# Optimization experiments

Hardware: AMD Instinct MI355X
Metric: run time of the kernel (lower is better)

## Reference

```python
import jax, jax.numpy as jnp
import numpy as np

N_NODES = 50000
N_EDGES = 800000
N_FEAT = 256


def setup_inputs() -> dict:
    key = jax.random.key(0)
    k_h, k_src, k_dst, k_w1, k_w2 = jax.random.split(key, 5)
    h = jax.random.normal(k_h, (N_NODES, N_FEAT), dtype=jnp.float32)
    src = jax.random.randint(k_src, (N_EDGES,), 0, N_NODES, dtype=jnp.int32)
    dst = jax.random.randint(k_dst, (N_EDGES,), 0, N_NODES, dtype=jnp.int32)
    # Kaiming-uniform-ish init like nn.Linear defaults
    b1 = 1.0 / np.sqrt(2 * N_FEAT)
    b2 = 1.0 / np.sqrt(N_FEAT)
    W1_w = jax.random.uniform(k_w1, (N_FEAT, 2 * N_FEAT), dtype=jnp.float32, minval=-b1, maxval=b1)
    W1_b = jnp.zeros((N_FEAT,), dtype=jnp.float32)
    W2_w = jax.random.uniform(k_w2, (1, N_FEAT), dtype=jnp.float32, minval=-b2, maxval=b2)
    W2_b = jnp.zeros((1,), dtype=jnp.float32)
    return {"h": h, "src": src, "dst": dst, "W1_w": W1_w, "W1_b": W1_b, "W2_w": W2_w, "W2_b": W2_b}


def reference(h, src, dst, W1_w, W1_b, W2_w, W2_b):
    # Gather per-edge endpoint features and concat along feature dim: [E, 2F]
    e = jnp.concatenate([h[src], h[dst]], axis=-1)
    # 2-layer MLP: Linear -> ReLU -> Linear, squeeze to per-edge score [E]
    hid = jax.nn.relu(e @ W1_w.T + W1_b)          # [E, F]
    score = (hid @ W2_w.T + W2_b)[:, 0]            # [E]
    return score
```

## Files before the change

### kernel.cpp

```cpp
#include <hip/hip_runtime.h>

#define F 256
#define TWO_F 512
#define BM 128
#define BN 128
#define BK 64
#define ASTR 72

typedef __attribute__((ext_vector_type(8))) short short8;
typedef __attribute__((ext_vector_type(4))) float float4v;

static __device__ __forceinline__ unsigned short f2bf(float f) {
    unsigned u = __float_as_uint(f);
    u += 0x7FFFu + ((u >> 16) & 1u);
    return (unsigned short)(u >> 16);
}
static __device__ __forceinline__ unsigned pack2(float lo, float hi) {
    unsigned a = __float_as_uint(lo) + 0x8000u;
    unsigned b = __float_as_uint(hi) + 0x8000u;
    return __builtin_amdgcn_perm(b, a, 0x07060302u);
}
static __device__ __forceinline__ float blo(unsigned u) { return __uint_as_float(u << 16); }
static __device__ __forceinline__ float rawf(unsigned u) { return __uint_as_float(u); }

__global__ void prep_w_kernel(const float* __restrict__ W1, unsigned short* __restrict__ Wb) {
    int i = blockIdx.x * blockDim.x + threadIdx.x;
    if (i >= TWO_F * F) return;
    int n = i >> 8;
    int k = i & 255;
    float v = W1[(n & 255) * TWO_F + ((n >> 8) << 8) + k];
    int kin_sw = ((k & 63) + (n & 7) * 8) & 63;
    Wb[n * F + (k & ~63) + kin_sw] = f2bf(v);
}

__global__ __launch_bounds__(256, 3) void gemm_kernel(
    const float* __restrict__ h, const unsigned short* __restrict__ Wb,
    const float* __restrict__ b1v, unsigned short* __restrict__ C, int M)
{
    __shared__ unsigned short sA[BM * ASTR];
    __shared__ unsigned short sB[BN * BK];

    const int ib = blockIdx.x;
    const int r8 = ib & 7;
    const int q  = ib >> 3;
    const int by = q & 3;
    const int bx = (q >> 2) * 8 + r8;
    const int bm = bx * BM;
    if (bm >= M) return;
    const int bn = by * BN;

    const int tid  = threadIdx.x;
    const int lane = tid & 63;
    const int wid  = tid >> 6;
    const int wm   = wid >> 1;
    const int wn   = wid & 1;

    const int ar = tid >> 1;
    const int ak = (tid & 1) * 32;
    int arow = bm + ar; if (arow > M - 1) arow = M - 1;
    const float* hrow = h + (size_t)arow * F + ak;

    const int brow0 = wid * 32;
    const int b_r   = lane >> 3;
    const int b_k   = (lane & 7) * 8;

    float4v acc[4][4];
    #pragma unroll
    for (int i = 0; i < 4; ++i)
        #pragma unroll
        for (int j = 0; j < 4; ++j) acc[i][j] = (float4v)(0.f);

    const int quad = lane >> 4;
    const int l15  = lane & 15;
    const int ksw  = (l15 & 7) * 8;

    for (int k0 = 0; k0 < F; k0 += BK) {
        #pragma unroll
        for (int p = 0; p < 4; ++p) {
            int r = brow0 + p * 8;
            const unsigned short* gp = Wb + (size_t)(bn + r + b_r) * F + k0 + b_k;
            __builtin_amdgcn_global_load_lds(
                (const __attribute__((address_space(1))) unsigned int*)gp,
                (__attribute__((address_space(3))) unsigned int*)&sB[r * BK],
                16, 0, 0);
        }

        const float* p = hrow + k0;
        #pragma unroll
        for (int half = 0; half < 2; ++half) {
            float4 a0 = *(const float4*)(p + half * 16 + 0);
            float4 a1 = *(const float4*)(p + half * 16 + 4);
            float4 a2 = *(const float4*)(p + half * 16 + 8);
            float4 a3 = *(const float4*)(p + half * 16 + 12);
            uint4 q0, q1;
            q0.x = pack2(a0.x, a0.y); q0.y = pack2(a0.z, a0.w);
            q0.z = pack2(a1.x, a1.y); q0.w = pack2(a1.z, a1.w);
            q1.x = pack2(a2.x, a2.y); q1.y = pack2(a2.z, a2.w);
            q1.z = pack2(a3.x, a3.y); q1.w = pack2(a3.z, a3.w);
            *(uint4*)&sA[ar * ASTR + ak + half * 16 + 0] = q0;
            *(uint4*)&sA[ar * ASTR + ak + half * 16 + 8] = q1;
        }
        __syncthreads();

        #pragma unroll
        for (int ks = 0; ks < 2; ++ks) {
            short8 afr[4], bfr[4];
            #pragma unroll
            for (int mt = 0; mt < 4; ++mt)
                afr[mt] = *(const short8*)&sA[(wm * 64 + mt * 16 + l15) * ASTR + ks * 32 + quad * 8];
            #pragma unroll
            for (int nt = 0; nt < 4; ++nt) {
                int koff = (ks * 32 + quad * 8 + ksw) & 63;
                bfr[nt] = *(const short8*)&sB[(wn * 64 + nt * 16 + l15) * BK + koff];
            }
            #pragma unroll
            for (int mt = 0; mt < 4; ++mt)
                #pragma unroll
                for (int nt = 0; nt < 4; ++nt)
                    acc[mt][nt] = __builtin_amdgcn_mfma_f32_16x16x32_bf16(
                        afr[mt], bfr[nt], acc[mt][nt], 0, 0, 0);
        }
        __syncthreads();
    }

    float bias[4];
    #pragma unroll
    for (int nt = 0; nt < 4; ++nt) {
        int n = bn + wn * 64 + nt * 16 + l15;
        bias[nt] = (n < F) ? b1v[n] : 0.f;
    }
    #pragma unroll
    for (int mt = 0; mt < 4; ++mt) {
        int gm0 = bm + wm * 64 + mt * 16 + quad * 4;
        #pragma unroll
        for (int rr = 0; rr < 4; ++rr) {
            int gm = gm0 + rr;
            if (gm < M) {
                unsigned short* cp = C + (size_t)gm * TWO_F + bn + wn * 64 + l15;
                #pragma unroll
                for (int nt = 0; nt < 4; ++nt)
                    cp[nt * 16] = f2bf(acc[mt][nt][rr] + bias[nt]);
            }
        }
    }
}

__global__ __launch_bounds__(256) void edge_kernel(
    const unsigned short* __restrict__ C,
    const int* __restrict__ src, const int* __restrict__ dst,
    const float* __restrict__ w2,
    const float* __restrict__ b2, float* __restrict__ out, int E)
{
    const int lane = threadIdx.x & 31;
    const int g = blockIdx.x * 8 + (threadIdx.x >> 5);
    const int e0 = g * 2;
    if (e0 >= E) return;
    const int s0 = src[e0], d0 = dst[e0];
    const int s1 = src[e0 + 1], d1 = dst[e0 + 1];

    uint4 av0 = *(const uint4*)(C + (size_t)s0 * TWO_F + lane * 8);
    uint4 bv0 = *(const uint4*)(C + (size_t)d0 * TWO_F + F + lane * 8);
    uint4 av1 = *(const uint4*)(C + (size_t)s1 * TWO_F + lane * 8);
    uint4 bv1 = *(const uint4*)(C + (size_t)d1 * TWO_F + F + lane * 8);
    float4 w0 = *(const float4*)(w2 + lane * 8);
    float4 w1 = *(const float4*)(w2 + lane * 8 + 4);

    float sum0, sum1;
    sum0  = w0.x * fmaxf(blo(av0.x) + blo(bv0.x), 0.f);
    sum0 += w0.y * fmaxf(rawf(av0.x) + rawf(bv0.x), 0.f);
    sum0 += w0.z * fmaxf(blo(av0.y) + blo(bv0.y), 0.f);
    sum0 += w0.w * fmaxf(rawf(av0.y) + rawf(bv0.y), 0.f);
    sum0 += w1.x * fmaxf(blo(av0.z) + blo(bv0.z), 0.f);
    sum0 += w1.y * fmaxf(rawf(av0.z) + rawf(bv0.z), 0.f);
    sum0 += w1.z * fmaxf(blo(av0.w) + blo(bv0.w), 0.f);
    sum0 += w1.w * fmaxf(rawf(av0.w) + rawf(bv0.w), 0.f);

    sum1  = w0.x * fmaxf(blo(av1.x) + blo(bv1.x), 0.f);
    sum1 += w0.y * fmaxf(rawf(av1.x) + rawf(bv1.x), 0.f);
    sum1 += w0.z * fmaxf(blo(av1.y) + blo(bv1.y), 0.f);
    sum1 += w0.w * fmaxf(rawf(av1.y) + rawf(bv1.y), 0.f);
    sum1 += w1.x * fmaxf(blo(av1.z) + blo(bv1.z), 0.f);
    sum1 += w1.y * fmaxf(rawf(av1.z) + rawf(bv1.z), 0.f);
    sum1 += w1.z * fmaxf(blo(av1.w) + blo(bv1.w), 0.f);
    sum1 += w1.w * fmaxf(rawf(av1.w) + rawf(bv1.w), 0.f);

    #pragma unroll
    for (int off = 16; off > 0; off >>= 1) {
        sum0 += __shfl_down(sum0, off, 32);
        sum1 += __shfl_down(sum1, off, 32);
    }

    if (lane == 0) {
        float b = b2[0];
        out[e0]     = sum0 + b;
        out[e0 + 1] = sum1 + b;
    }
}

extern "C" void kernel_launch(void* const* d_in, const int* in_sizes, int n_in,
                              void* d_out, int out_size, void* d_ws, size_t ws_size,
                              hipStream_t stream) {
    const float* h    = (const float*)d_in[0];
    const int*   src  = (const int*)d_in[1];
    const int*   dst  = (const int*)d_in[2];
    const float* W1_w = (const float*)d_in[3];
    const float* W1_b = (const float*)d_in[4];
    const float* W2_w = (const float*)d_in[5];
    const float* W2_b = (const float*)d_in[6];
    float* out = (float*)d_out;

    const int M = in_sizes[0] / F;
    const int E = in_sizes[1];

    unsigned short* Wb = (unsigned short*)d_ws;
    unsigned short* C  = (unsigned short*)((char*)d_ws + 512 * 1024);

    prep_w_kernel<<<(TWO_F * F + 255) / 256, 256, 0, stream>>>(W1_w, Wb);

    int nbx = ((M + BM - 1) / BM + 7) / 8 * 8;
    gemm_kernel<<<nbx * 4, 256, 0, stream>>>(h, Wb, W1_b, C, M);

    edge_kernel<<<(E / 2 + 7) / 8, 256, 0, stream>>>(C, src, dst, W2_w, W2_b, out, E);
}
```

Before: 241.3 us.

## Pre-convert h to swizzled bf16 and load A tiles via global_load_lds; widen edge batching

Adds a prep kernel that converts h to bf16 in a swizzled layout, so the GEMM can stream A tiles straight into LDS with global_load_lds like B, instead of loading fp32 into registers, packing and storing to LDS on every iteration. The edge kernel now handles four edges per 32-lane group, with vectorized index loads and a float4 output store, so more gathers are in flight. The cost is an extra kernel launch plus a full fp32 read and bf16 write of h, and the four-edge vector access assumes E is a multiple of 4.

```diff
diff --git a/kernel.cpp b/kernel.cpp
--- a/kernel.cpp
+++ b/kernel.cpp
@@ -5,7 +5,6 @@
 #define BM 128
 #define BN 128
 #define BK 64
-#define ASTR 72
 
 typedef __attribute__((ext_vector_type(8))) short short8;
 typedef __attribute__((ext_vector_type(4))) float float4v;
@@ -33,11 +32,24 @@
     Wb[n * F + (k & ~63) + kin_sw] = f2bf(v);
 }
 
+__global__ __launch_bounds__(256) void prep_h_kernel(
+    const float* __restrict__ h, unsigned short* __restrict__ hb, int M)
+{
+    int i = blockIdx.x * blockDim.x + threadIdx.x;
+    if (i >= M * 128) return;
+    int m = i >> 7;
+    int kp = (i & 127) * 2;
+    float2 v = *(const float2*)(h + (size_t)m * F + kp);
+    unsigned pk = pack2(v.x, v.y);
+    int ksw = ((kp & 63) + (m & 7) * 8) & 63;
+    *(unsigned*)(hb + (size_t)m * F + (kp & ~63) + ksw) = pk;
+}
+
 __global__ __launch_bounds__(256, 3) void gemm_kernel(
-    const float* __restrict__ h, const unsigned short* __restrict__ Wb,
+    const unsigned short* __restrict__ hb, const unsigned short* __restrict__ Wb,
     const float* __restrict__ b1v, unsigned short* __restrict__ C, int M)
 {
-    __shared__ unsigned short sA[BM * ASTR];
+    __shared__ unsigned short sA[BM * BK];
     __shared__ unsigned short sB[BN * BK];
 
     const int ib = blockIdx.x;
@@ -55,14 +67,9 @@
     const int wm   = wid >> 1;
     const int wn   = wid & 1;
 
-    const int ar = tid >> 1;
-    const int ak = (tid & 1) * 32;
-    int arow = bm + ar; if (arow > M - 1) arow = M - 1;
-    const float* hrow = h + (size_t)arow * F + ak;
-
-    const int brow0 = wid * 32;
-    const int b_r   = lane >> 3;
-    const int b_k   = (lane & 7) * 8;
+    const int row0 = wid * 32;
+    const int st_r = lane >> 3;
+    const int st_k = (lane & 7) * 8;
 
     float4v acc[4][4];
     #pragma unroll
@@ -72,47 +79,36 @@
 
     const int quad = lane >> 4;
     const int l15  = lane & 15;
-    const int ksw  = (l15 & 7) * 8;
+    const int rot  = (l15 & 7) * 8;
 
     for (int k0 = 0; k0 < F; k0 += BK) {
         #pragma unroll
         for (int p = 0; p < 4; ++p) {
-            int r = brow0 + p * 8;
-            const unsigned short* gp = Wb + (size_t)(bn + r + b_r) * F + k0 + b_k;
+            int r = row0 + p * 8;
+            int am = bm + r + st_r; if (am > M - 1) am = M - 1;
+            const unsigned short* ga = hb + (size_t)am * F + k0 + st_k;
             __builtin_amdgcn_global_load_lds(
-                (const __attribute__((address_space(1))) unsigned int*)gp,
+                (const __attribute__((address_space(1))) unsigned int*)ga,
+                (__attribute__((address_space(3))) unsigned int*)&sA[r * BK],
+                16, 0, 0);
+            const unsigned short* gb = Wb + (size_t)(bn + r + st_r) * F + k0 + st_k;
+            __builtin_amdgcn_global_load_lds(
+                (const __attribute__((address_space(1))) unsigned int*)gb,
                 (__attribute__((address_space(3))) unsigned int*)&sB[r * BK],
                 16, 0, 0);
         }
-
-        const float* p = hrow + k0;
-        #pragma unroll
-        for (int half = 0; half < 2; ++half) {
-            float4 a0 = *(const float4*)(p + half * 16 + 0);
-            float4 a1 = *(const float4*)(p + half * 16 + 4);
-            float4 a2 = *(const float4*)(p + half * 16 + 8);
-            float4 a3 = *(const float4*)(p + half * 16 + 12);
-            uint4 q0, q1;
-            q0.x = pack2(a0.x, a0.y); q0.y = pack2(a0.z, a0.w);
-            q0.z = pack2(a1.x, a1.y); q0.w = pack2(a1.z, a1.w);
-            q1.x = pack2(a2.x, a2.y); q1.y = pack2(a2.z, a2.w);
-            q1.z = pack2(a3.x, a3.y); q1.w = pack2(a3.z, a3.w);
-            *(uint4*)&sA[ar * ASTR + ak + half * 16 + 0] = q0;
-            *(uint4*)&sA[ar * ASTR + ak + half * 16 + 8] = q1;
-        }
         __syncthreads();
 
         #pragma unroll
         for (int ks = 0; ks < 2; ++ks) {
+            const int koff = (ks * 32 + quad * 8 + rot) & 63;
             short8 afr[4], bfr[4];
             #pragma unroll
             for (int mt = 0; mt < 4; ++mt)
-                afr[mt] = *(const short8*)&sA[(wm * 64 + mt * 16 + l15) * ASTR + ks * 32 + quad * 8];
+                afr[mt] = *(const short8*)&sA[(wm * 64 + mt * 16 + l15) * BK + koff];
             #pragma unroll
-            for (int nt = 0; nt < 4; ++nt) {
-                int koff = (ks * 32 + quad * 8 + ksw) & 63;
+            for (int nt = 0; nt < 4; ++nt)
                 bfr[nt] = *(const short8*)&sB[(wn * 64 + nt * 16 + l15) * BK + koff];
-            }
             #pragma unroll
             for (int mt = 0; mt < 4; ++mt)
                 #pragma unroll
@@ -153,47 +149,52 @@
 {
     const int lane = threadIdx.x & 31;
     const int g = blockIdx.x * 8 + (threadIdx.x >> 5);
-    const int e0 = g * 2;
+    const int e0 = g * 4;
     if (e0 >= E) return;
-    const int s0 = src[e0], d0 = dst[e0];
-    const int s1 = src[e0 + 1], d1 = dst[e0 + 1];
-
-    uint4 av0 = *(const uint4*)(C + (size_t)s0 * TWO_F + lane * 8);
-    uint4 bv0 = *(const uint4*)(C + (size_t)d0 * TWO_F + F + lane * 8);
-    uint4 av1 = *(const uint4*)(C + (size_t)s1 * TWO_F + lane * 8);
-    uint4 bv1 = *(const uint4*)(C + (size_t)d1 * TWO_F + F + lane * 8);
+    int4 sv = *(const int4*)(src + e0);
+    int4 dv = *(const int4*)(dst + e0);
+
+    const unsigned short* Ca = C + lane * 8;
+    const unsigned short* Cb = C + F + lane * 8;
+    uint4 a0 = *(const uint4*)(Ca + (size_t)sv.x * TWO_F);
+    uint4 b0 = *(const uint4*)(Cb + (size_t)dv.x * TWO_F);
+    uint4 a1 = *(const uint4*)(Ca + (size_t)sv.y * TWO_F);
+    uint4 b1 = *(const uint4*)(Cb + (size_t)dv.y * TWO_F);
+    uint4 a2 = *(const uint4*)(Ca + (size_t)sv.z * TWO_F);
+    uint4 b2v = *(const uint4*)(Cb + (size_t)dv.z * TWO_F);
+    uint4 a3 = *(const uint4*)(Ca + (size_t)sv.w * TWO_F);
+    uint4 b3 = *(const uint4*)(Cb + (size_t)dv.w * TWO_F);
     float4 w0 = *(const float4*)(w2 + lane * 8);
     float4 w1 = *(const float4*)(w2 + lane * 8 + 4);
 
-    float sum0, sum1;
-    sum0  = w0.x * fmaxf(blo(av0.x) + blo(bv0.x), 0.f);
-    sum0 += w0.y * fmaxf(rawf(av0.x) + rawf(bv0.x), 0.f);
-    sum0 += w0.z * fmaxf(blo(av0.y) + blo(bv0.y), 0.f);
-    sum0 += w0.w * fmaxf(rawf(av0.y) + rawf(bv0.y), 0.f);
-    sum0 += w1.x * fmaxf(blo(av0.z) + blo(bv0.z), 0.f);
-    sum0 += w1.y * fmaxf(rawf(av0.z) + rawf(bv0.z), 0.f);
-    sum0 += w1.z * fmaxf(blo(av0.w) + blo(bv0.w), 0.f);
-    sum0 += w1.w * fmaxf(rawf(av0.w) + rawf(bv0.w), 0.f);
-
-    sum1  = w0.x * fmaxf(blo(av1.x) + blo(bv1.x), 0.f);
-    sum1 += w0.y * fmaxf(rawf(av1.x) + rawf(bv1.x), 0.f);
-    sum1 += w0.z * fmaxf(blo(av1.y) + blo(bv1.y), 0.f);
-    sum1 += w0.w * fmaxf(rawf(av1.y) + rawf(bv1.y), 0.f);
-    sum1 += w1.x * fmaxf(blo(av1.z) + blo(bv1.z), 0.f);
-    sum1 += w1.y * fmaxf(rawf(av1.z) + rawf(bv1.z), 0.f);
-    sum1 += w1.z * fmaxf(blo(av1.w) + blo(bv1.w), 0.f);
-    sum1 += w1.w * fmaxf(rawf(av1.w) + rawf(bv1.w), 0.f);
+#define ESUM(s, av, bv)                                   \
+    s  = w0.x * fmaxf(blo(av.x) + blo(bv.x), 0.f);        \
+    s += w0.y * fmaxf(rawf(av.x) + rawf(bv.x), 0.f);      \
+    s += w0.z * fmaxf(blo(av.y) + blo(bv.y), 0.f);        \
+    s += w0.w * fmaxf(rawf(av.y) + rawf(bv.y), 0.f);      \
+    s += w1.x * fmaxf(blo(av.z) + blo(bv.z), 0.f);        \
+    s += w1.y * fmaxf(rawf(av.z) + rawf(bv.z), 0.f);      \
+    s += w1.z * fmaxf(blo(av.w) + blo(bv.w), 0.f);        \
+    s += w1.w * fmaxf(rawf(av.w) + rawf(bv.w), 0.f);
+
+    float sum0, sum1, sum2, sum3;
+    ESUM(sum0, a0, b0)
+    ESUM(sum1, a1, b1)
+    ESUM(sum2, a2, b2v)
+    ESUM(sum3, a3, b3)
+#undef ESUM
 
     #pragma unroll
     for (int off = 16; off > 0; off >>= 1) {
         sum0 += __shfl_down(sum0, off, 32);
         sum1 += __shfl_down(sum1, off, 32);
+        sum2 += __shfl_down(sum2, off, 32);
+        sum3 += __shfl_down(sum3, off, 32);
     }
 
     if (lane == 0) {
         float b = b2[0];
-        out[e0]     = sum0 + b;
-        out[e0 + 1] = sum1 + b;
+        *(float4*)(out + e0) = make_float4(sum0 + b, sum1 + b, sum2 + b, sum3 + b);
     }
 }
 
@@ -213,12 +214,14 @@
     const int E = in_sizes[1];
 
     unsigned short* Wb = (unsigned short*)d_ws;
-    unsigned short* C  = (unsigned short*)((char*)d_ws + 512 * 1024);
+    unsigned short* hb = (unsigned short*)((char*)d_ws + 512 * 1024);
+    unsigned short* C  = (unsigned short*)((char*)d_ws + 512 * 1024 + 26 * 1024 * 1024);
 
     prep_w_kernel<<<(TWO_F * F + 255) / 256, 256, 0, stream>>>(W1_w, Wb);
+    prep_h_kernel<<<(M * 128 + 255) / 256, 256, 0, stream>>>(h, hb, M);
 
     int nbx = ((M + BM - 1) / BM + 7) / 8 * 8;
-    gemm_kernel<<<nbx * 4, 256, 0, stream>>>(h, Wb, W1_b, C, M);
-
-    edge_kernel<<<(E / 2 + 7) / 8, 256, 0, stream>>>(C, src, dst, W2_w, W2_b, out, E);
-}
+    gemm_kernel<<<nbx * 4, 256, 0, stream>>>(hb, Wb, W1_b, C, M);
+
+    edge_kernel<<<(E / 4 + 7) / 8, 256, 0, stream>>>(C, src, dst, W2_w, W2_b, out, E);
+}
```

Result: faster. 230.4 us (-4.5%).

## Hold weight tile in registers and stream A from global without LDS

Applied to the files above, without the earlier changes.

The GEMM kernel drops its shared-memory tiling. Each wave now keeps its full 64-column by 256-K slice of bf16 weights in registers (32 short8 fragments) and walks eight 16-row M tiles. It reads h directly from global memory into MFMA A-fragments with no barriers. The grid shrinks to two N-halves per 128-row chunk, and the weight prep no longer swizzles. This removes LDS traffic and syncs, at the cost of heavy register pressure (launch bounds reduced to 2), redundant h reads across the four waves, and lower occupancy.

```diff
diff --git a/kernel.cpp b/kernel.cpp
--- a/kernel.cpp
+++ b/kernel.cpp
@@ -2,10 +2,6 @@
 
 #define F 256
 #define TWO_F 512
-#define BM 128
-#define BN 128
-#define BK 64
-#define ASTR 72
 
 typedef __attribute__((ext_vector_type(8))) short short8;
 typedef __attribute__((ext_vector_type(4))) float float4v;
@@ -28,118 +24,71 @@
     if (i >= TWO_F * F) return;
     int n = i >> 8;
     int k = i & 255;
-    float v = W1[(n & 255) * TWO_F + ((n >> 8) << 8) + k];
-    int kin_sw = ((k & 63) + (n & 7) * 8) & 63;
-    Wb[n * F + (k & ~63) + kin_sw] = f2bf(v);
+    Wb[i] = f2bf(W1[(n & 255) * TWO_F + ((n >> 8) << 8) + k]);
 }
 
-__global__ __launch_bounds__(256, 3) void gemm_kernel(
+__global__ __launch_bounds__(256, 2) void gemm_kernel(
     const float* __restrict__ h, const unsigned short* __restrict__ Wb,
     const float* __restrict__ b1v, unsigned short* __restrict__ C, int M)
 {
-    __shared__ unsigned short sA[BM * ASTR];
-    __shared__ unsigned short sB[BN * BK];
+    const int tid  = threadIdx.x;
+    const int lane = tid & 63;
+    const int wv   = tid >> 6;
+    const int quad = lane >> 4;
+    const int l15  = lane & 15;
 
     const int ib = blockIdx.x;
-    const int r8 = ib & 7;
-    const int q  = ib >> 3;
-    const int by = q & 3;
-    const int bx = (q >> 2) * 8 + r8;
-    const int bm = bx * BM;
-    if (bm >= M) return;
-    const int bn = by * BN;
+    const int mchunk = (ib >> 4) * 8 + (ib & 7);
+    const int by = (ib >> 3) & 1;
+    const int m0 = mchunk * 128;
+    if (m0 >= M) return;
+    const int nbase = by * 256 + wv * 64;
 
-    const int tid  = threadIdx.x;
-    const int lane = tid & 63;
-    const int wid  = tid >> 6;
-    const int wm   = wid >> 1;
-    const int wn   = wid & 1;
-
-    const int ar = tid >> 1;
-    const int ak = (tid & 1) * 32;
-    int arow = bm + ar; if (arow > M - 1) arow = M - 1;
-    const float* hrow = h + (size_t)arow * F + ak;
-
-    const int brow0 = wid * 32;
-    const int b_r   = lane >> 3;
-    const int b_k   = (lane & 7) * 8;
-
-    float4v acc[4][4];
+    short8 bfr[4][8];
     #pragma unroll
-    for (int i = 0; i < 4; ++i)
+    for (int nt = 0; nt < 4; ++nt) {
+        const unsigned short* bp = Wb + (size_t)(nbase + nt * 16 + l15) * F + quad * 8;
         #pragma unroll
-        for (int j = 0; j < 4; ++j) acc[i][j] = (float4v)(0.f);
-
-    const int quad = lane >> 4;
-    const int l15  = lane & 15;
-    const int ksw  = (l15 & 7) * 8;
-
-    for (int k0 = 0; k0 < F; k0 += BK) {
-        #pragma unroll
-        for (int p = 0; p < 4; ++p) {
-            int r = brow0 + p * 8;
-            const unsigned short* gp = Wb + (size_t)(bn + r + b_r) * F + k0 + b_k;
-            __builtin_amdgcn_global_load_lds(
-                (const __attribute__((address_space(1))) unsigned int*)gp,
-                (__attribute__((address_space(3))) unsigned int*)&sB[r * BK],
-                16, 0, 0);
-        }
-
-        const float* p = hrow + k0;
-        #pragma unroll
-        for (int half = 0; half < 2; ++half) {
-            float4 a0 = *(const float4*)(p + half * 16 + 0);
-            float4 a1 = *(const float4*)(p + half * 16 + 4);
-            float4 a2 = *(const float4*)(p + half * 16 + 8);
-            float4 a3 = *(const float4*)(p + half * 16 + 12);
-            uint4 q0, q1;
-            q0.x = pack2(a0.x, a0.y); q0.y = pack2(a0.z, a0.w);
-            q0.z = pack2(a1.x, a1.y); q0.w = pack2(a1.z, a1.w);
-            q1.x = pack2(a2.x, a2.y); q1.y = pack2(a2.z, a2.w);
-            q1.z = pack2(a3.x, a3.y); q1.w = pack2(a3.z, a3.w);
-            *(uint4*)&sA[ar * ASTR + ak + half * 16 + 0] = q0;
-            *(uint4*)&sA[ar * ASTR + ak + half * 16 + 8] = q1;
-        }
-        __syncthreads();
-
-        #pragma unroll
-        for (int ks = 0; ks < 2; ++ks) {
-            short8 afr[4], bfr[4];
-            #pragma unroll
-            for (int mt = 0; mt < 4; ++mt)
-                afr[mt] = *(const short8*)&sA[(wm * 64 + mt * 16 + l15) * ASTR + ks * 32 + quad * 8];
-            #pragma unroll
-            for (int nt = 0; nt < 4; ++nt) {
-                int koff = (ks * 32 + quad * 8 + ksw) & 63;
-                bfr[nt] = *(const short8*)&sB[(wn * 64 + nt * 16 + l15) * BK + koff];
-            }
-            #pragma unroll
-            for (int mt = 0; mt < 4; ++mt)
-                #pragma unroll
-                for (int nt = 0; nt < 4; ++nt)
-                    acc[mt][nt] = __builtin_amdgcn_mfma_f32_16x16x32_bf16(
-                        afr[mt], bfr[nt], acc[mt][nt], 0, 0, 0);
-        }
-        __syncthreads();
+        for (int ks = 0; ks < 8; ++ks)
+            bfr[nt][ks] = *(const short8*)(bp + ks * 32);
     }
 
     float bias[4];
     #pragma unroll
-    for (int nt = 0; nt < 4; ++nt) {
-        int n = bn + wn * 64 + nt * 16 + l15;
-        bias[nt] = (n < F) ? b1v[n] : 0.f;
-    }
-    #pragma unroll
-    for (int mt = 0; mt < 4; ++mt) {
-        int gm0 = bm + wm * 64 + mt * 16 + quad * 4;
+    for (int nt = 0; nt < 4; ++nt)
+        bias[nt] = (by == 0) ? b1v[nbase + nt * 16 + l15] : 0.f;
+
+    for (int t = 0; t < 8; ++t) {
+        const int mt0 = m0 + t * 16;
+        int arow = mt0 + l15; if (arow > M - 1) arow = M - 1;
+        const float* ap = h + (size_t)arow * F + quad * 8;
+
+        float4v acc[4];
+        acc[0] = acc[1] = acc[2] = acc[3] = (float4v)(0.f);
+
         #pragma unroll
-        for (int rr = 0; rr < 4; ++rr) {
-            int gm = gm0 + rr;
+        for (int ks = 0; ks < 8; ++ks) {
+            float4 lo = *(const float4*)(ap + ks * 32);
+            float4 hi = *(const float4*)(ap + ks * 32 + 4);
+            union { unsigned u[4]; short8 s; } a;
+            a.u[0] = pack2(lo.x, lo.y);
+            a.u[1] = pack2(lo.z, lo.w);
+            a.u[2] = pack2(hi.x, hi.y);
+            a.u[3] = pack2(hi.z, hi.w);
+            #pragma unroll
+            for (int nt = 0; nt < 4; ++nt)
+                acc[nt] = __builtin_amdgcn_mfma_f32_16x16x32_bf16(
+                    a.s, bfr[nt][ks], acc[nt], 0, 0, 0);
+        }
+
+        #pragma unroll
+        for (int r = 0; r < 4; ++r) {
+            int gm = mt0 + quad * 4 + r;
             if (gm < M) {
-                unsigned short* cp = C + (size_t)gm * TWO_F + bn + wn * 64 + l15;
+                unsigned short* cp = C + (size_t)gm * TWO_F + nbase + l15;
                 #pragma unroll
                 for (int nt = 0; nt < 4; ++nt)
-                    cp[nt * 16] = f2bf(acc[mt][nt][rr] + bias[nt]);
+                    cp[nt * 16] = f2bf(acc[nt][r] + bias[nt]);
             }
         }
     }
@@ -217,8 +166,8 @@
 
     prep_w_kernel<<<(TWO_F * F + 255) / 256, 256, 0, stream>>>(W1_w, Wb);
 
-    int nbx = ((M + BM - 1) / BM + 7) / 8 * 8;
-    gemm_kernel<<<nbx * 4, 256, 0, stream>>>(h, Wb, W1_b, C, M);
+    int nchunks = ((M + 127) / 128 + 7) / 8 * 8;
+    gemm_kernel<<<nchunks * 2, 256, 0, stream>>>(h, Wb, W1_b, C, M);
 
     edge_kernel<<<(E / 2 + 7) / 8, 256, 0, stream>>>(C, src, dst, W2_w, W2_b, out, E);
 }
```

Measured after the change: 274.5 us. 13.8% more time.

## Pre-convert h to swizzled bf16 and stream A tiles via direct global-to-LDS loads

Applied to the files above, without the earlier changes.

A prep kernel now converts h to bf16 in a swizzled layout alongside the weight preparation. The GEMM then loads both A and B tiles with global_load_lds instead of doing fp32 loads and an in-register conversion per tile. The N tile shrinks from 128 to 64 with occupancy raised to 4, so each block computes a smaller tile and the grid doubles. The aim is to cut A-side conversion overhead and raise occupancy, at the cost of an extra round trip of h through memory and re-reading each A tile for twice as many N blocks.

```diff
diff --git a/kernel.cpp b/kernel.cpp
--- a/kernel.cpp
+++ b/kernel.cpp
@@ -3,9 +3,8 @@
 #define F 256
 #define TWO_F 512
 #define BM 128
-#define BN 128
+#define BN 64
 #define BK 64
-#define ASTR 72
 
 typedef __attribute__((ext_vector_type(8))) short short8;
 typedef __attribute__((ext_vector_type(4))) float float4v;
@@ -23,28 +22,40 @@
 static __device__ __forceinline__ float blo(unsigned u) { return __uint_as_float(u << 16); }
 static __device__ __forceinline__ float rawf(unsigned u) { return __uint_as_float(u); }
 
-__global__ void prep_w_kernel(const float* __restrict__ W1, unsigned short* __restrict__ Wb) {
+__global__ __launch_bounds__(256) void prep_kernel(
+    const float* __restrict__ h, const float* __restrict__ W1,
+    unsigned short* __restrict__ hb, unsigned short* __restrict__ Wb, int M)
+{
     int i = blockIdx.x * blockDim.x + threadIdx.x;
-    if (i >= TWO_F * F) return;
-    int n = i >> 8;
-    int k = i & 255;
-    float v = W1[(n & 255) * TWO_F + ((n >> 8) << 8) + k];
-    int kin_sw = ((k & 63) + (n & 7) * 8) & 63;
-    Wb[n * F + (k & ~63) + kin_sw] = f2bf(v);
-}
-
-__global__ __launch_bounds__(256, 3) void gemm_kernel(
-    const float* __restrict__ h, const unsigned short* __restrict__ Wb,
+    if (i < M * 128) {
+        int m = i >> 7;
+        int kp = (i & 127) * 2;
+        float2 v = *(const float2*)(h + (size_t)m * F + kp);
+        unsigned pk = pack2(v.x, v.y);
+        int ksw = ((kp & 63) + (m & 7) * 8) & 63;
+        *(unsigned*)(hb + (size_t)m * F + (kp & ~63) + ksw) = pk;
+    }
+    if (i < TWO_F * F) {
+        int n = i >> 8;
+        int k = i & 255;
+        float v = W1[(n & 255) * TWO_F + ((n >> 8) << 8) + k];
+        int kin_sw = ((k & 63) + (n & 7) * 8) & 63;
+        Wb[n * F + (k & ~63) + kin_sw] = f2bf(v);
+    }
+}
+
+__global__ __launch_bounds__(256, 4) void gemm_kernel(
+    const unsigned short* __restrict__ hb, const unsigned short* __restrict__ Wb,
     const float* __restrict__ b1v, unsigned short* __restrict__ C, int M)
 {
-    __shared__ unsigned short sA[BM * ASTR];
+    __shared__ unsigned short sA[BM * BK];
     __shared__ unsigned short sB[BN * BK];
 
     const int ib = blockIdx.x;
     const int r8 = ib & 7;
     const int q  = ib >> 3;
-    const int by = q & 3;
-    const int bx = (q >> 2) * 8 + r8;
+    const int by = q & 7;
+    const int bx = (q >> 3) * 8 + r8;
     const int bm = bx * BM;
     if (bm >= M) return;
     const int bn = by * BN;
@@ -52,69 +63,52 @@
     const int tid  = threadIdx.x;
     const int lane = tid & 63;
     const int wid  = tid >> 6;
-    const int wm   = wid >> 1;
-    const int wn   = wid & 1;
-
-    const int ar = tid >> 1;
-    const int ak = (tid & 1) * 32;
-    int arow = bm + ar; if (arow > M - 1) arow = M - 1;
-    const float* hrow = h + (size_t)arow * F + ak;
-
-    const int brow0 = wid * 32;
-    const int b_r   = lane >> 3;
-    const int b_k   = (lane & 7) * 8;
-
-    float4v acc[4][4];
-    #pragma unroll
-    for (int i = 0; i < 4; ++i)
-        #pragma unroll
-        for (int j = 0; j < 4; ++j) acc[i][j] = (float4v)(0.f);
-
+    const int st_r = lane >> 3;
+    const int st_k = (lane & 7) * 8;
     const int quad = lane >> 4;
     const int l15  = lane & 15;
-    const int ksw  = (l15 & 7) * 8;
+    const int rot  = (l15 & 7) * 8;
+
+    float4v acc[2][4];
+    #pragma unroll
+    for (int i = 0; i < 2; ++i)
+        #pragma unroll
+        for (int j = 0; j < 4; ++j) acc[i][j] = (float4v)(0.f);
 
     for (int k0 = 0; k0 < F; k0 += BK) {
         #pragma unroll
         for (int p = 0; p < 4; ++p) {
-            int r = brow0 + p * 8;
-            const unsigned short* gp = Wb + (size_t)(bn + r + b_r) * F + k0 + b_k;
+            int r = wid * 32 + p * 8;
+            int am = bm + r + st_r; if (am > M - 1) am = M - 1;
+            const unsigned short* ga = hb + (size_t)am * F + k0 + st_k;
             __builtin_amdgcn_global_load_lds(
-                (const __attribute__((address_space(1))) unsigned int*)gp,
+                (const __attribute__((address_space(1))) unsigned int*)ga,
+                (__attribute__((address_space(3))) unsigned int*)&sA[r * BK],
+                16, 0, 0);
+        }
+        #pragma unroll
+        for (int p = 0; p < 2; ++p) {
+            int r = wid * 16 + p * 8;
+            const unsigned short* gb = Wb + (size_t)(bn + r + st_r) * F + k0 + st_k;
+            __builtin_amdgcn_global_load_lds(
+                (const __attribute__((address_space(1))) unsigned int*)gb,
                 (__attribute__((address_space(3))) unsigned int*)&sB[r * BK],
                 16, 0, 0);
         }
-
-        const float* p = hrow + k0;
-        #pragma unroll
-        for (int half = 0; half < 2; ++half) {
-            float4 a0 = *(const float4*)(p + half * 16 + 0);
-            float4 a1 = *(const float4*)(p + half * 16 + 4);
-            float4 a2 = *(const float4*)(p + half * 16 + 8);
-            float4 a3 = *(const float4*)(p + half * 16 + 12);
-            uint4 q0, q1;
-            q0.x = pack2(a0.x, a0.y); q0.y = pack2(a0.z, a0.w);
-            q0.z = pack2(a1.x, a1.y); q0.w = pack2(a1.z, a1.w);
-            q1.x = pack2(a2.x, a2.y); q1.y = pack2(a2.z, a2.w);
-            q1.z = pack2(a3.x, a3.y); q1.w = pack2(a3.z, a3.w);
-            *(uint4*)&sA[ar * ASTR + ak + half * 16 + 0] = q0;
-            *(uint4*)&sA[ar * ASTR + ak + half * 16 + 8] = q1;
-        }
         __syncthreads();
 
         #pragma unroll
         for (int ks = 0; ks < 2; ++ks) {
-            short8 afr[4], bfr[4];
+            const int koff = (ks * 32 + quad * 8 + rot) & 63;
+            short8 afr[2], bfr[4];
             #pragma unroll
-            for (int mt = 0; mt < 4; ++mt)
-                afr[mt] = *(const short8*)&sA[(wm * 64 + mt * 16 + l15) * ASTR + ks * 32 + quad * 8];
+            for (int mt = 0; mt < 2; ++mt)
+                afr[mt] = *(const short8*)&sA[(wid * 32 + mt * 16 + l15) * BK + koff];
             #pragma unroll
-            for (int nt = 0; nt < 4; ++nt) {
-                int koff = (ks * 32 + quad * 8 + ksw) & 63;
-                bfr[nt] = *(const short8*)&sB[(wn * 64 + nt * 16 + l15) * BK + koff];
-            }
+            for (int nt = 0; nt < 4; ++nt)
+                bfr[nt] = *(const short8*)&sB[(nt * 16 + l15) * BK + koff];
             #pragma unroll
-            for (int mt = 0; mt < 4; ++mt)
+            for (int mt = 0; mt < 2; ++mt)
                 #pragma unroll
                 for (int nt = 0; nt < 4; ++nt)
                     acc[mt][nt] = __builtin_amdgcn_mfma_f32_16x16x32_bf16(
@@ -126,17 +120,17 @@
     float bias[4];
     #pragma unroll
     for (int nt = 0; nt < 4; ++nt) {
-        int n = bn + wn * 64 + nt * 16 + l15;
+        int n = bn + nt * 16 + l15;
         bias[nt] = (n < F) ? b1v[n] : 0.f;
     }
     #pragma unroll
-    for (int mt = 0; mt < 4; ++mt) {
-        int gm0 = bm + wm * 64 + mt * 16 + quad * 4;
+    for (int mt = 0; mt < 2; ++mt) {
+        int gm0 = bm + wid * 32 + mt * 16 + quad * 4;
         #pragma unroll
         for (int rr = 0; rr < 4; ++rr) {
             int gm = gm0 + rr;
             if (gm < M) {
-                unsigned short* cp = C + (size_t)gm * TWO_F + bn + wn * 64 + l15;
+                unsigned short* cp = C + (size_t)gm * TWO_F + bn + l15;
                 #pragma unroll
                 for (int nt = 0; nt < 4; ++nt)
                     cp[nt * 16] = f2bf(acc[mt][nt][rr] + bias[nt]);
@@ -213,12 +207,14 @@
     const int E = in_sizes[1];
 
     unsigned short* Wb = (unsigned short*)d_ws;
-    unsigned short* C  = (unsigned short*)((char*)d_ws + 512 * 1024);
-
-    prep_w_kernel<<<(TWO_F * F + 255) / 256, 256, 0, stream>>>(W1_w, Wb);
+    unsigned short* hb = (unsigned short*)((char*)d_ws + 512 * 1024);
+    unsigned short* C  = (unsigned short*)((char*)d_ws + 512 * 1024 + 26 * 1024 * 1024);
+
+    int prep_threads = M * 128 > TWO_F * F ? M * 128 : TWO_F * F;
+    prep_kernel<<<(prep_threads + 255) / 256, 256, 0, stream>>>(h, W1_w, hb, Wb, M);
 
     int nbx = ((M + BM - 1) / BM + 7) / 8 * 8;
-    gemm_kernel<<<nbx * 4, 256, 0, stream>>>(h, Wb, W1_b, C, M);
+    gemm_kernel<<<nbx * 8, 256, 0, stream>>>(hb, Wb, W1_b, C, M);
 
     edge_kernel<<<(E / 2 + 7) / 8, 256, 0, stream>>>(C, src, dst, W2_w, W2_b, out, E);
 }
```

Result: faster. 226.7 us (-6.0%).
